# Kernel tuning notes

Measured on AMD Instinct MI355X. Metric: run time of the kernel, lower is better.

Reference implementation:

```python
import jax, jax.numpy as jnp
import numpy as np

N_HEADS = 16


def setup_inputs() -> dict:
    key = jax.random.key(0)
    k1, k2 = jax.random.split(key)
    bs, width, length = 8, 3 * N_HEADS * 64, 1024  # C=64 per head
    qkv = jax.random.normal(k1, (bs, width, length), dtype=jnp.float32)
    mask = jax.random.uniform(k2, (bs, length), dtype=jnp.float32)
    return {"qkv": qkv, "mask": mask}


def reference(qkv, mask):
    bs, width, length = qkv.shape
    ch = width // (3 * N_HEADS)
    q, k, v = jnp.split(qkv, 3, axis=1)
    # view(bs*H, ch, T): head index is inner (b*H + h ordering)
    q = q.reshape(bs * N_HEADS, ch, length)
    k = k.reshape(bs * N_HEADS, ch, length)
    v = v.reshape(bs * N_HEADS, ch, length)
    scale = 1.0 / jnp.sqrt(jnp.sqrt(jnp.asarray(ch, dtype=qkv.dtype)))
    # [bs*H, T, T] score matrix
    weight = jnp.einsum('bct,bcs->bts', q * scale, k * scale)
    # torch mask.repeat(n_heads, 1) tiles the batch dim -> jnp.tile
    m = jnp.tile(mask, (N_HEADS, 1))[:, None, :]  # [bs*H, 1, T]
    weight = weight * m
    weight = jax.nn.softmax(weight.astype(jnp.float32), axis=-1).astype(weight.dtype)
    a = jnp.einsum('bts,bcs->bct', weight, v)  # [bs*H, ch, T]
    return a.reshape(bs, N_HEADS * ch, length)
```

## Files before the change

### kernel.cpp

```cpp
#include <hip/hip_runtime.h>
#include <stdint.h>
#include <math.h>

typedef float  f32x4  __attribute__((ext_vector_type(4)));
typedef __bf16 bf16x8 __attribute__((ext_vector_type(8)));
typedef __bf16 bf16x4 __attribute__((ext_vector_type(4)));

#define MFMA16(a, b, c) __builtin_amdgcn_mfma_f32_16x16x32_bf16((a), (b), (c), 0, 0, 0)
#define EXP2(x) __builtin_amdgcn_exp2f(x)

static constexpr int kT = 1024;

static constexpr int kTileEl = 4096;
static constexpr size_t kTensorEl    = (size_t)128 * 16 * kTileEl;
static constexpr size_t kTensorBytes = kTensorEl * 2;

static constexpr int kLS = 72;

__device__ inline void async16(const void* g, void* l) {
  __builtin_amdgcn_global_load_lds(
      (const __attribute__((address_space(1))) void*)g,
      (__attribute__((address_space(3))) void*)l, 16, 0, 0);
}

__global__ __launch_bounds__(256, 8)
void prepass(const float* __restrict__ qkv, const float* __restrict__ mask,
             __bf16* __restrict__ kh, __bf16* __restrict__ vh)
{
  __shared__ float ts[64 * 65];
  const int tid = threadIdx.x;
  const int bid = blockIdx.x, bh = bid >> 4, tile = bid & 15;
  const int b = bh >> 4, h = bh & 15, t0 = tile * 64;
  const float* __restrict__ kb = qkv + (size_t)(b * 3072 + 1024 + h * 64) * kT;
  const float* __restrict__ vb = qkv + (size_t)(b * 3072 + 2048 + h * 64) * kT;
  const float* __restrict__ mrow = mask + (size_t)(h & 7) * kT;
  const size_t tbase = ((size_t)bh * 16 + tile) * kTileEl;

  const int t4   = (tid & 15) * 4;
  const int crow = tid >> 4;
  const f32x4 m4 = *(const f32x4*)&mrow[t0 + t4];
  #pragma unroll
  for (int i = 0; i < 4; ++i) {
    const int c = i * 16 + crow;
    f32x4 k4 = *(const f32x4*)&kb[(size_t)c * kT + t0 + t4];
    k4 *= m4;
    *(f32x4*)&ts[c * 65 + t4] = k4;
  }
  __syncthreads();

  #pragma unroll
  for (int i = 0; i < 2; ++i) {
    const int p = i * 256 + tid;
    const int chunk = p >> 6, pl = p & 63;
    const int vc  = (chunk >> 1) * 16 + (pl & 15);
    const int vs0 = (chunk & 1) * 32 + (pl >> 4) * 8;
    const f32x4 va  = *(const f32x4*)&vb[(size_t)vc * kT + t0 + vs0];
    const f32x4 vbq = *(const f32x4*)&vb[(size_t)vc * kT + t0 + vs0 + 4];
    const int ks  = (chunk >> 1) * 16 + (pl & 15);
    const int kc0 = (chunk & 1) * 32 + (pl >> 4) * 8;
    bf16x8 k8, v8;
    #pragma unroll
    for (int j = 0; j < 8; ++j) k8[j] = (__bf16)ts[(kc0 + j) * 65 + ks];
    #pragma unroll
    for (int j = 0; j < 4; ++j) { v8[j] = (__bf16)va[j]; v8[4 + j] = (__bf16)vbq[j]; }
    *(bf16x8*)&kh[tbase + (size_t)p * 8] = k8;
    *(bf16x8*)&vh[tbase + (size_t)p * 8] = v8;
  }
}

__global__ __launch_bounds__(256, 3)
void attn_main(const float* __restrict__ qkv,
               const __bf16* __restrict__ kh, const __bf16* __restrict__ vh,
               float* __restrict__ out)
{
  __shared__ __align__(16) char smem[49152];

  const int tid  = threadIdx.x;
  const int lane = tid & 63;
  const int wave = tid >> 6;
  const int quad = lane >> 4;
  const int l15  = lane & 15;

  const int bid = blockIdx.x;
  const int bh  = bid & 127;
  const int tp  = bid >> 7;
  const int b   = bh >> 4;
  const int h   = bh & 15;
  const int t0  = tp * 128;
  const size_t hbase = (size_t)bh * 16;

  bf16x8 qh[2][2], ql[2][2];
  {
    float* ts = (float*)smem;
    const float* __restrict__ qb = qkv + (size_t)(b * 3072 + h * 64) * kT;
    const int t4   = (tid & 15) * 4;
    const int crow = tid >> 4;
    const int trow = wave * 16 + l15;
    #pragma unroll
    for (int half = 0; half < 2; ++half) {
      const int tq0 = t0 + half * 64;
      #pragma unroll
      for (int i = 0; i < 4; ++i) {
        const int c = i * 16 + crow;
        f32x4 q4 = *(const f32x4*)&qb[(size_t)c * kT + tq0 + t4];
        q4 *= 0.18033688f;
        *(f32x4*)&ts[c * 65 + t4] = q4;
      }
      __syncthreads();
      #pragma unroll
      for (int kc = 0; kc < 2; ++kc) {
        bf16x8 hf, lf;
        #pragma unroll
        for (int j = 0; j < 8; ++j) {
          float q = ts[(kc * 32 + quad * 8 + j) * 65 + trow];
          __bf16 hi = (__bf16)q;
          hf[j] = hi;
          lf[j] = (__bf16)(q - (float)hi);
        }
        qh[half][kc] = hf;
        ql[half][kc] = lf;
      }
      __syncthreads();
    }
  }

  {
    const char* g = (const char*)(kh + hbase * kTileEl) + (size_t)lane * 16;
    for (int i = wave; i < 16; i += 4) async16(g + i * 1024, smem + i * 1024);
  }

  f32x4 O0[4], O1[4];
  #pragma unroll
  for (int cc = 0; cc < 4; ++cc) {
    O0[cc] = (f32x4){0.f, 0.f, 0.f, 0.f};
    O1[cc] = (f32x4){0.f, 0.f, 0.f, 0.f};
  }
  f32x4 la0 = (f32x4){0.f, 0.f, 0.f, 0.f};
  f32x4 la1 = (f32x4){0.f, 0.f, 0.f, 0.f};

  char* sP0 = smem + 32768 + wave * 4096;
  char* sP1 = sP0 + 2048;
  const int pwr = (l15 << 4) + ((quad & 1) << 3) + ((quad >> 1) << 8);

  for (int p = 0; p < 8; ++p) {
    __syncthreads();

    if (p < 7) {
      const char* g = (const char*)(kh + (hbase + 2 * (p + 1)) * kTileEl) + (size_t)lane * 16;
      char* l = smem + ((p + 1) & 1) * 16384;
      for (int i = wave; i < 16; i += 4) async16(g + i * 1024, l + i * 1024);
    }

    #pragma unroll
    for (int u = 0; u < 2; ++u) {
      const __bf16* __restrict__ vt  = vh + (hbase + 2 * p + u) * kTileEl;
      const __bf16* __restrict__ sKt = (const __bf16*)(smem + (p & 1) * 16384 + u * 8192);

      bf16x8 vf0[4], vf1[4];
      #pragma unroll
      for (int cc = 0; cc < 4; ++cc)
        vf0[cc] = *(const bf16x8*)&vt[(size_t)(cc * 2) * 512 + lane * 8];

      #pragma unroll
      for (int sc = 0; sc < 4; ++sc) {
        bf16x8 k0 = *(const bf16x8*)&sKt[(size_t)(sc * 2) * 512 + lane * 8];
        bf16x8 k1 = *(const bf16x8*)&sKt[(size_t)(sc * 2 + 1) * 512 + lane * 8];
        f32x4 a0 = (f32x4){0.f, 0.f, 0.f, 0.f};
        f32x4 a1 = (f32x4){0.f, 0.f, 0.f, 0.f};
        a0 = MFMA16(k0, ql[0][0], a0);
        a1 = MFMA16(k0, ql[1][0], a1);
        a0 = MFMA16(k0, qh[0][0], a0);
        a1 = MFMA16(k0, qh[1][0], a1);
        a0 = MFMA16(k1, ql[0][1], a0);
        a1 = MFMA16(k1, ql[1][1], a1);
        a0 = MFMA16(k1, qh[0][1], a0);
        a1 = MFMA16(k1, qh[1][1], a1);
        f32x4 e0, e1;
        #pragma unroll
        for (int r = 0; r < 4; ++r) {
          e0[r] = EXP2(a0[r]);
          e1[r] = EXP2(a1[r]);
        }
        la0 += e0;
        la1 += e1;
        bf16x4 p0, p1;
        #pragma unroll
        for (int r = 0; r < 4; ++r) {
          p0[r] = (__bf16)e0[r];
          p1[r] = (__bf16)e1[r];
        }
        const int po = ((sc >> 1) << 10) + ((sc & 1) << 9) + pwr;
        *(bf16x4*)(sP0 + po) = p0;
        *(bf16x4*)(sP1 + po) = p1;
      }

      #pragma unroll
      for (int cc = 0; cc < 4; ++cc)
        vf1[cc] = *(const bf16x8*)&vt[(size_t)(cc * 2 + 1) * 512 + lane * 8];

      bf16x8 pb00 = *(const bf16x8*)(sP0 + lane * 16);
      bf16x8 pb01 = *(const bf16x8*)(sP0 + 1024 + lane * 16);
      bf16x8 pb10 = *(const bf16x8*)(sP1 + lane * 16);
      bf16x8 pb11 = *(const bf16x8*)(sP1 + 1024 + lane * 16);

      #pragma unroll
      for (int cc = 0; cc < 4; ++cc) {
        O0[cc] = MFMA16(vf0[cc], pb00, O0[cc]);
        O1[cc] = MFMA16(vf0[cc], pb10, O1[cc]);
        O0[cc] = MFMA16(vf1[cc], pb01, O0[cc]);
        O1[cc] = MFMA16(vf1[cc], pb11, O1[cc]);
      }
    }
  }

  float ls0 = la0[0] + la0[1] + la0[2] + la0[3];
  float ls1 = la1[0] + la1[1] + la1[2] + la1[3];
  ls0 += __shfl_xor(ls0, 16);
  ls0 += __shfl_xor(ls0, 32);
  ls1 += __shfl_xor(ls1, 16);
  ls1 += __shfl_xor(ls1, 32);
  const float inv0 = 1.0f / ls0;
  const float inv1 = 1.0f / ls1;

  const int tcol = t0 + wave * 16 + l15;
  float* __restrict__ obase = out + (size_t)b * (1024 * 1024) + (size_t)(h * 64) * kT;
  #pragma unroll
  for (int cc = 0; cc < 4; ++cc) {
    #pragma unroll
    for (int r = 0; r < 4; ++r) {
      const int c = cc * 16 + quad * 4 + r;
      obase[(size_t)c * kT + tcol]      = O0[cc][r] * inv0;
      obase[(size_t)c * kT + tcol + 64] = O1[cc][r] * inv1;
    }
  }
}

__global__ __launch_bounds__(256, 2)
void attn_fused(const float* __restrict__ qkv, const float* __restrict__ mask,
                float* __restrict__ out)
{
  __shared__ __align__(16) __bf16 Ahi[64 * kLS];
  __shared__ __align__(16) __bf16 Alo[64 * kLS];
  __shared__ __align__(16) __bf16 Vhi[64 * kLS];
  __shared__ __align__(16) __bf16 Vlo[64 * kLS];
  __shared__ __align__(16) __bf16 Phi[64 * kLS];
  __shared__ __align__(16) __bf16 Plo[64 * kLS];
  __shared__ __align__(16) float  ms[64];

  const int tid  = threadIdx.x;
  const int lane = tid & 63;
  const int wave = tid >> 6;
  const int quad = lane >> 4;
  const int l15  = lane & 15;

  const int bid = blockIdx.x;
  const int bh  = bid >> 4;
  const int tb  = bid & 15;
  const int b   = bh >> 4;
  const int h   = bh & 15;
  const int t0  = tb * 64;

  const float* __restrict__ qbase = qkv + (size_t)(b * 3072 + h * 64) * kT;
  const float* __restrict__ kbase = qkv + (size_t)(b * 3072 + 1024 + h * 64) * kT;
  const float* __restrict__ vbase = qkv + (size_t)(b * 3072 + 2048 + h * 64) * kT;
  const float* __restrict__ mrow  = mask + (size_t)(h & 7) * kT;

  const int sl = tid & 63;
  const int cg = tid >> 6;

  #pragma unroll
  for (int i = 0; i < 16; ++i) {
    const int c = cg * 16 + i;
    float v  = qbase[(size_t)c * kT + t0 + sl] * 0.125f;
    __bf16 hi = (__bf16)v;
    Ahi[sl * kLS + c] = hi;
    Alo[sl * kLS + c] = (__bf16)(v - (float)hi);
  }
  __syncthreads();

  bf16x8 qh[2], ql[2];
  {
    const int row = (wave * 16 + l15) * kLS;
    #pragma unroll
    for (int kc = 0; kc < 2; ++kc) {
      qh[kc] = *(const bf16x8*)&Ahi[row + kc * 32 + quad * 8];
      ql[kc] = *(const bf16x8*)&Alo[row + kc * 32 + quad * 8];
    }
  }
  __syncthreads();

  f32x4 O[4];
  #pragma unroll
  for (int cc = 0; cc < 4; ++cc) O[cc] = (f32x4){0.f, 0.f, 0.f, 0.f};
  float m_run = -__builtin_inff();
  float l_run = 0.f;

  for (int s0 = 0; s0 < kT; s0 += 64) {
    #pragma unroll
    for (int i = 0; i < 16; ++i) {
      const int c = cg * 16 + i;
      float kv   = kbase[(size_t)c * kT + s0 + sl];
      __bf16 khi = (__bf16)kv;
      Ahi[sl * kLS + c] = khi;
      Alo[sl * kLS + c] = (__bf16)(kv - (float)khi);
      float vv   = vbase[(size_t)c * kT + s0 + sl];
      __bf16 vhi = (__bf16)vv;
      Vhi[c * kLS + sl] = vhi;
      Vlo[c * kLS + sl] = (__bf16)(vv - (float)vhi);
    }
    if (tid < 64) ms[tid] = mrow[s0 + tid];
    __syncthreads();

    f32x4 S[4];
    #pragma unroll
    for (int sc = 0; sc < 4; ++sc) {
      f32x4 acc = (f32x4){0.f, 0.f, 0.f, 0.f};
      #pragma unroll
      for (int kc = 0; kc < 2; ++kc) {
        const int off = (sc * 16 + l15) * kLS + kc * 32 + quad * 8;
        bf16x8 kh8 = *(const bf16x8*)&Ahi[off];
        bf16x8 kl8 = *(const bf16x8*)&Alo[off];
        acc = MFMA16(kh8, ql[kc], acc);
        acc = MFMA16(kl8, qh[kc], acc);
        acc = MFMA16(kh8, qh[kc], acc);
      }
      S[sc] = acc;
    }

    float x[16];
    float tmax = -__builtin_inff();
    #pragma unroll
    for (int sc = 0; sc < 4; ++sc) {
      f32x4 mv = *(const f32x4*)&ms[sc * 16 + quad * 4];
      #pragma unroll
      for (int r = 0; r < 4; ++r) {
        float xv = S[sc][r] * mv[r];
        x[sc * 4 + r] = xv;
        tmax = fmaxf(tmax, xv);
      }
    }
    tmax = fmaxf(tmax, __shfl_xor(tmax, 16));
    tmax = fmaxf(tmax, __shfl_xor(tmax, 32));
    const float mnew  = fmaxf(m_run, tmax);
    const float alpha = __expf(m_run - mnew);
    float tsum = 0.f;
    #pragma unroll
    for (int i = 0; i < 16; ++i) {
      float p = __expf(x[i] - mnew);
      x[i] = p;
      tsum += p;
    }
    tsum += __shfl_xor(tsum, 16);
    tsum += __shfl_xor(tsum, 32);
    l_run = l_run * alpha + tsum;
    m_run = mnew;
    #pragma unroll
    for (int cc = 0; cc < 4; ++cc) O[cc] = O[cc] * alpha;

    const int prow = (wave * 16 + l15) * kLS;
    #pragma unroll
    for (int sc = 0; sc < 4; ++sc) {
      bf16x4 ph, pl;
      #pragma unroll
      for (int r = 0; r < 4; ++r) {
        float p   = x[sc * 4 + r];
        __bf16 hi = (__bf16)p;
        ph[r] = hi;
        pl[r] = (__bf16)(p - (float)hi);
      }
      *(bf16x4*)&Phi[prow + sc * 16 + quad * 4] = ph;
      *(bf16x4*)&Plo[prow + sc * 16 + quad * 4] = pl;
    }
    __syncthreads();

    bf16x8 pbh[2], pbl[2];
    #pragma unroll
    for (int kc = 0; kc < 2; ++kc) {
      pbh[kc] = *(const bf16x8*)&Phi[prow + kc * 32 + quad * 8];
      pbl[kc] = *(const bf16x8*)&Plo[prow + kc * 32 + quad * 8];
    }
    #pragma unroll
    for (int cc = 0; cc < 4; ++cc) {
      #pragma unroll
      for (int kc = 0; kc < 2; ++kc) {
        const int off = (cc * 16 + l15) * kLS + kc * 32 + quad * 8;
        bf16x8 v8 = *(const bf16x8*)&Vhi[off];
        bf16x8 w8 = *(const bf16x8*)&Vlo[off];
        O[cc] = MFMA16(v8, pbl[kc], O[cc]);
        O[cc] = MFMA16(w8, pbh[kc], O[cc]);
        O[cc] = MFMA16(v8, pbh[kc], O[cc]);
      }
    }
    __syncthreads();
  }

  const float inv  = 1.0f / l_run;
  const int   tcol = t0 + wave * 16 + l15;
  float* __restrict__ obase = out + (size_t)b * (1024 * 1024) + (size_t)(h * 64) * kT;
  #pragma unroll
  for (int cc = 0; cc < 4; ++cc) {
    #pragma unroll
    for (int r = 0; r < 4; ++r) {
      const int c = cc * 16 + quad * 4 + r;
      obase[(size_t)c * kT + tcol] = O[cc][r] * inv;
    }
  }
}

extern "C" void kernel_launch(void* const* d_in, const int* in_sizes, int n_in,
                              void* d_out, int out_size, void* d_ws, size_t ws_size,
                              hipStream_t stream)
{
  const float* qkv  = (const float*)d_in[0];
  const float* mask = (const float*)d_in[1];
  float* out = (float*)d_out;
  (void)in_sizes; (void)n_in; (void)out_size;

  if (ws_size >= 2 * kTensorBytes) {
    char* w = (char*)d_ws;
    __bf16* kh = (__bf16*)(w + 0 * kTensorBytes);
    __bf16* vh = (__bf16*)(w + 1 * kTensorBytes);
    prepass<<<dim3(2048), dim3(256), 0, stream>>>(qkv, mask, kh, vh);
    attn_main<<<dim3(1024), dim3(256), 0, stream>>>(qkv, kh, vh, out);
  } else {
    attn_fused<<<dim3(2048), dim3(256), 0, stream>>>(qkv, mask, out);
  }
}
```

Measured before the change: 204.9 us.

## Load K directly from global instead of async LDS staging; coalesce V in prepass

The main attention loop stops staging K tiles through LDS with async global_load_lds double buffering and the per-iteration block barriers. Each wave now reads K fragments straight from global memory (L2), and LDS shrinks to just the per-wave P buffers, which lets occupancy rise to 4 blocks. The prepass also reads V with coalesced row loads and transposes it through a second LDS tile. The cost is that global-load latency is no longer hidden by explicit prefetching, and each wave re-fetches K from cache.

```diff
diff --git a/kernel.cpp b/kernel.cpp
--- a/kernel.cpp
+++ b/kernel.cpp
@@ -17,17 +17,12 @@
 
 static constexpr int kLS = 72;
 
-__device__ inline void async16(const void* g, void* l) {
-  __builtin_amdgcn_global_load_lds(
-      (const __attribute__((address_space(1))) void*)g,
-      (__attribute__((address_space(3))) void*)l, 16, 0, 0);
-}
-
-__global__ __launch_bounds__(256, 8)
+__global__ __launch_bounds__(256, 4)
 void prepass(const float* __restrict__ qkv, const float* __restrict__ mask,
              __bf16* __restrict__ kh, __bf16* __restrict__ vh)
 {
-  __shared__ float ts[64 * 65];
+  __shared__ float tsK[64 * 65];
+  __shared__ float tsV[64 * 65];
   const int tid = threadIdx.x;
   const int bid = blockIdx.x, bh = bid >> 4, tile = bid & 15;
   const int b = bh >> 4, h = bh & 15, t0 = tile * 64;
@@ -43,8 +38,10 @@
   for (int i = 0; i < 4; ++i) {
     const int c = i * 16 + crow;
     f32x4 k4 = *(const f32x4*)&kb[(size_t)c * kT + t0 + t4];
+    f32x4 v4 = *(const f32x4*)&vb[(size_t)c * kT + t0 + t4];
     k4 *= m4;
-    *(f32x4*)&ts[c * 65 + t4] = k4;
+    *(f32x4*)&tsK[c * 65 + t4] = k4;
+    *(f32x4*)&tsV[c * 65 + t4] = v4;
   }
   __syncthreads();
 
@@ -52,28 +49,25 @@
   for (int i = 0; i < 2; ++i) {
     const int p = i * 256 + tid;
     const int chunk = p >> 6, pl = p & 63;
-    const int vc  = (chunk >> 1) * 16 + (pl & 15);
-    const int vs0 = (chunk & 1) * 32 + (pl >> 4) * 8;
-    const f32x4 va  = *(const f32x4*)&vb[(size_t)vc * kT + t0 + vs0];
-    const f32x4 vbq = *(const f32x4*)&vb[(size_t)vc * kT + t0 + vs0 + 4];
-    const int ks  = (chunk >> 1) * 16 + (pl & 15);
+    const int rr  = (chunk >> 1) * 16 + (pl & 15);
     const int kc0 = (chunk & 1) * 32 + (pl >> 4) * 8;
     bf16x8 k8, v8;
     #pragma unroll
-    for (int j = 0; j < 8; ++j) k8[j] = (__bf16)ts[(kc0 + j) * 65 + ks];
-    #pragma unroll
-    for (int j = 0; j < 4; ++j) { v8[j] = (__bf16)va[j]; v8[4 + j] = (__bf16)vbq[j]; }
+    for (int j = 0; j < 8; ++j) {
+      k8[j] = (__bf16)tsK[(kc0 + j) * 65 + rr];
+      v8[j] = (__bf16)tsV[rr * 65 + kc0 + j];
+    }
     *(bf16x8*)&kh[tbase + (size_t)p * 8] = k8;
     *(bf16x8*)&vh[tbase + (size_t)p * 8] = v8;
   }
 }
 
-__global__ __launch_bounds__(256, 3)
+__global__ __launch_bounds__(256, 4)
 void attn_main(const float* __restrict__ qkv,
                const __bf16* __restrict__ kh, const __bf16* __restrict__ vh,
                float* __restrict__ out)
 {
-  __shared__ __align__(16) char smem[49152];
+  __shared__ __align__(16) char smem[16640];
 
   const int tid  = threadIdx.x;
   const int lane = tid & 63;
@@ -124,11 +118,6 @@
     }
   }
 
-  {
-    const char* g = (const char*)(kh + hbase * kTileEl) + (size_t)lane * 16;
-    for (int i = wave; i < 16; i += 4) async16(g + i * 1024, smem + i * 1024);
-  }
-
   f32x4 O0[4], O1[4];
   #pragma unroll
   for (int cc = 0; cc < 4; ++cc) {
@@ -138,78 +127,66 @@
   f32x4 la0 = (f32x4){0.f, 0.f, 0.f, 0.f};
   f32x4 la1 = (f32x4){0.f, 0.f, 0.f, 0.f};
 
-  char* sP0 = smem + 32768 + wave * 4096;
+  char* sP0 = smem + wave * 4096;
   char* sP1 = sP0 + 2048;
   const int pwr = (l15 << 4) + ((quad & 1) << 3) + ((quad >> 1) << 8);
 
-  for (int p = 0; p < 8; ++p) {
-    __syncthreads();
-
-    if (p < 7) {
-      const char* g = (const char*)(kh + (hbase + 2 * (p + 1)) * kTileEl) + (size_t)lane * 16;
-      char* l = smem + ((p + 1) & 1) * 16384;
-      for (int i = wave; i < 16; i += 4) async16(g + i * 1024, l + i * 1024);
-    }
-
-    #pragma unroll
-    for (int u = 0; u < 2; ++u) {
-      const __bf16* __restrict__ vt  = vh + (hbase + 2 * p + u) * kTileEl;
-      const __bf16* __restrict__ sKt = (const __bf16*)(smem + (p & 1) * 16384 + u * 8192);
-
-      bf16x8 vf0[4], vf1[4];
-      #pragma unroll
-      for (int cc = 0; cc < 4; ++cc)
-        vf0[cc] = *(const bf16x8*)&vt[(size_t)(cc * 2) * 512 + lane * 8];
-
-      #pragma unroll
-      for (int sc = 0; sc < 4; ++sc) {
-        bf16x8 k0 = *(const bf16x8*)&sKt[(size_t)(sc * 2) * 512 + lane * 8];
-        bf16x8 k1 = *(const bf16x8*)&sKt[(size_t)(sc * 2 + 1) * 512 + lane * 8];
-        f32x4 a0 = (f32x4){0.f, 0.f, 0.f, 0.f};
-        f32x4 a1 = (f32x4){0.f, 0.f, 0.f, 0.f};
-        a0 = MFMA16(k0, ql[0][0], a0);
-        a1 = MFMA16(k0, ql[1][0], a1);
-        a0 = MFMA16(k0, qh[0][0], a0);
-        a1 = MFMA16(k0, qh[1][0], a1);
-        a0 = MFMA16(k1, ql[0][1], a0);
-        a1 = MFMA16(k1, ql[1][1], a1);
-        a0 = MFMA16(k1, qh[0][1], a0);
-        a1 = MFMA16(k1, qh[1][1], a1);
-        f32x4 e0, e1;
-        #pragma unroll
-        for (int r = 0; r < 4; ++r) {
-          e0[r] = EXP2(a0[r]);
-          e1[r] = EXP2(a1[r]);
-        }
-        la0 += e0;
-        la1 += e1;
-        bf16x4 p0, p1;
-        #pragma unroll
-        for (int r = 0; r < 4; ++r) {
-          p0[r] = (__bf16)e0[r];
-          p1[r] = (__bf16)e1[r];
-        }
-        const int po = ((sc >> 1) << 10) + ((sc & 1) << 9) + pwr;
-        *(bf16x4*)(sP0 + po) = p0;
-        *(bf16x4*)(sP1 + po) = p1;
-      }
-
-      #pragma unroll
-      for (int cc = 0; cc < 4; ++cc)
-        vf1[cc] = *(const bf16x8*)&vt[(size_t)(cc * 2 + 1) * 512 + lane * 8];
-
-      bf16x8 pb00 = *(const bf16x8*)(sP0 + lane * 16);
-      bf16x8 pb01 = *(const bf16x8*)(sP0 + 1024 + lane * 16);
-      bf16x8 pb10 = *(const bf16x8*)(sP1 + lane * 16);
-      bf16x8 pb11 = *(const bf16x8*)(sP1 + 1024 + lane * 16);
-
-      #pragma unroll
-      for (int cc = 0; cc < 4; ++cc) {
-        O0[cc] = MFMA16(vf0[cc], pb00, O0[cc]);
-        O1[cc] = MFMA16(vf0[cc], pb10, O1[cc]);
-        O0[cc] = MFMA16(vf1[cc], pb01, O0[cc]);
-        O1[cc] = MFMA16(vf1[cc], pb11, O1[cc]);
-      }
+  for (int st = 0; st < 16; ++st) {
+    const __bf16* __restrict__ kt = kh + (hbase + st) * kTileEl;
+    const __bf16* __restrict__ vt = vh + (hbase + st) * kTileEl;
+
+    bf16x8 vf0[4], vf1[4];
+    #pragma unroll
+    for (int cc = 0; cc < 4; ++cc)
+      vf0[cc] = *(const bf16x8*)&vt[(size_t)(cc * 2) * 512 + lane * 8];
+    #pragma unroll
+    for (int cc = 0; cc < 4; ++cc)
+      vf1[cc] = *(const bf16x8*)&vt[(size_t)(cc * 2 + 1) * 512 + lane * 8];
+
+    #pragma unroll
+    for (int sc = 0; sc < 4; ++sc) {
+      bf16x8 k0 = *(const bf16x8*)&kt[(size_t)(sc * 2) * 512 + lane * 8];
+      bf16x8 k1 = *(const bf16x8*)&kt[(size_t)(sc * 2 + 1) * 512 + lane * 8];
+      f32x4 a0 = (f32x4){0.f, 0.f, 0.f, 0.f};
+      f32x4 a1 = (f32x4){0.f, 0.f, 0.f, 0.f};
+      a0 = MFMA16(k0, ql[0][0], a0);
+      a1 = MFMA16(k0, ql[1][0], a1);
+      a0 = MFMA16(k0, qh[0][0], a0);
+      a1 = MFMA16(k0, qh[1][0], a1);
+      a0 = MFMA16(k1, ql[0][1], a0);
+      a1 = MFMA16(k1, ql[1][1], a1);
+      a0 = MFMA16(k1, qh[0][1], a0);
+      a1 = MFMA16(k1, qh[1][1], a1);
+      f32x4 e0, e1;
+      #pragma unroll
+      for (int r = 0; r < 4; ++r) {
+        e0[r] = EXP2(a0[r]);
+        e1[r] = EXP2(a1[r]);
+      }
+      la0 += e0;
+      la1 += e1;
+      bf16x4 p0, p1;
+      #pragma unroll
+      for (int r = 0; r < 4; ++r) {
+        p0[r] = (__bf16)e0[r];
+        p1[r] = (__bf16)e1[r];
+      }
+      const int po = ((sc >> 1) << 10) + ((sc & 1) << 9) + pwr;
+      *(bf16x4*)(sP0 + po) = p0;
+      *(bf16x4*)(sP1 + po) = p1;
+    }
+
+    bf16x8 pb00 = *(const bf16x8*)(sP0 + lane * 16);
+    bf16x8 pb01 = *(const bf16x8*)(sP0 + 1024 + lane * 16);
+    bf16x8 pb10 = *(const bf16x8*)(sP1 + lane * 16);
+    bf16x8 pb11 = *(const bf16x8*)(sP1 + 1024 + lane * 16);
+
+    #pragma unroll
+    for (int cc = 0; cc < 4; ++cc) {
+      O0[cc] = MFMA16(vf0[cc], pb00, O0[cc]);
+      O1[cc] = MFMA16(vf0[cc], pb10, O1[cc]);
+      O0[cc] = MFMA16(vf1[cc], pb01, O0[cc]);
+      O1[cc] = MFMA16(vf1[cc], pb11, O1[cc]);
     }
   }
 
```

After: 218.4 us. 6.6% more time.
